# Kernel tuning notes

Hardware: AMD Instinct MI355X
Metric: run time of the kernel (lower is better)

The kernel has to match this reference:

```python
import jax, jax.numpy as jnp
import numpy as np

B, N, D, K = 8, 2048, 256, 8192


def setup_inputs() -> dict:
    key = jax.random.key(0)
    k1, k2 = jax.random.split(key)
    x = jax.random.normal(k1, (B, N, D), dtype=jnp.float32)          # encoder output z_e (identity encoder)
    codebook = jax.random.normal(k2, (K, D), dtype=jnp.float32)      # nn.Parameter(codebook_size, codebook_dim)
    return {"x": x, "codebook": codebook}


def reference(x, codebook):
    z_e = x  # identity encoder
    # Squared Euclidean distances via matmul expansion: ||z||^2 - 2 z.c^T + ||c||^2 -> (B, N, K)
    z2 = jnp.sum(z_e * z_e, axis=-1, keepdims=True)                   # (B, N, 1)
    c2 = jnp.sum(codebook * codebook, axis=-1)                        # (K,)
    cross = jnp.einsum('bnd,kd->bnk', z_e, codebook)                  # (B, N, K)
    distances = z2 - 2.0 * cross + c2                                 # (B, N, K)
    indices = jnp.argmin(distances, axis=-1)                          # (B, N) int
    z_q = codebook[indices]                                           # gather -> (B, N, D)
    x_recon = z_q  # identity decoder
    return (x_recon, z_e, z_q, indices)
```

## Files before the change

kernel.cpp:

```cpp
#include <hip/hip_runtime.h>
#include <stdint.h>


#define M_ROWS 16384
#define D_DIM  256
#define K_CB   8192
#define NSPLIT 16
#define CHUNK  64
#define EPS 20.0f

typedef float f32x4 __attribute__((ext_vector_type(4)));
typedef int   int4v __attribute__((ext_vector_type(4)));
typedef int   int8v __attribute__((ext_vector_type(8)));

__device__ __forceinline__ uint32_t umin32(uint32_t a, uint32_t b) { return a < b ? a : b; }
__device__ __forceinline__ uint32_t umax32(uint32_t a, uint32_t b) { return a > b ? a : b; }

__device__ __forceinline__ void gld_lds16(const void* g, void* l) {
  __builtin_amdgcn_global_load_lds((__attribute__((address_space(1))) void*)g,
                                   (__attribute__((address_space(3))) void*)l,
                                   16, 0, 0);
}

__device__ __forceinline__ float rtne3(float f) {
  uint32_t u = __float_as_uint(f);
  u = (u + 0x0007FFFFu + ((u >> 20) & 1u)) & 0xFFF00000u;
  return __uint_as_float(u);
}

__device__ __forceinline__ uint32_t fp8x4(const f32x4 v) {
  int p = __builtin_amdgcn_cvt_pk_fp8_f32(rtne3(v[0]), rtne3(v[1]), 0, false);
  p = __builtin_amdgcn_cvt_pk_fp8_f32(rtne3(v[2]), rtne3(v[3]), p, true);
  return (uint32_t)p;
}

__global__ __launch_bounds__(256) void prep(const float* __restrict__ x,
                                            const float* __restrict__ cb,
                                            uint8_t* __restrict__ Ap,
                                            uint8_t* __restrict__ Bp,
                                            float* __restrict__ c2s,
                                            float* __restrict__ out_ze) {
  const int w = threadIdx.x >> 6, lane = threadIdx.x & 63;
  if (blockIdx.x < M_ROWS / 4) {
    const int row = blockIdx.x * 4 + w;
    const f32x4 v = *(const f32x4*)(x + (size_t)row * D_DIM + lane * 4);
    *(uint32_t*)(Ap + (size_t)row * D_DIM + lane * 4) = fp8x4(v);
    *(f32x4*)(out_ze + (size_t)row * D_DIM + lane * 4) = v;
  } else {
    const int row = (blockIdx.x - M_ROWS / 4) * 4 + w;
    const f32x4 v = *(const f32x4*)(cb + (size_t)row * D_DIM + lane * 4);
    *(uint32_t*)(Bp + (size_t)row * D_DIM + lane * 4) = fp8x4(v);
    double s = 0.0;
#pragma unroll
    for (int t = 0; t < 4; ++t) s += (double)v[t] * (double)v[t];
#pragma unroll
    for (int m = 1; m < 64; m <<= 1) s += __shfl_xor(s, m, 64);
    if (lane == 0) c2s[row] = (float)s + 1024.0f;
  }
}

__global__ __launch_bounds__(256, 3) void vq_main(const uint8_t* __restrict__ Ap,
                                                  const uint8_t* __restrict__ Bp,
                                                  const float* __restrict__ c2s,
                                                  uint4* __restrict__ part) {
  __shared__ uint8_t Bs[2][CHUNK * D_DIM];

  const int w    = threadIdx.x >> 6;
  const int lane = threadIdx.x & 63;
  const int fr   = lane & 15;
  const int fq   = lane >> 4;

  const int rowBase = blockIdx.x * 128 + w * 32;
  const int colBase = blockIdx.y * 512;

  int8v af[2][2];
  {
    const uint8_t* ab = Ap + (size_t)(rowBase + fr) * D_DIM + fq * 32;
#pragma unroll
    for (int i = 0; i < 2; ++i)
#pragma unroll
      for (int kh = 0; kh < 2; ++kh)
        af[i][kh] = *(const int8v*)(ab + (size_t)(i * 16) * D_DIM + kh * 128);
  }

  uint32_t t1[2][4], t2[2][4], t3[2][4], t4[2][4];
#pragma unroll
  for (int i = 0; i < 2; ++i)
#pragma unroll
    for (int r = 0; r < 4; ++r) {
      t1[i][r] = 0x7f7ffe00u; t2[i][r] = 0x7f7ffe00u;
      t3[i][r] = 0x7f7ffe00u; t4[i][r] = 0x7f7ffe00u;
    }

  const int dRow = lane >> 4;
  const int dChk = lane & 15;
#define STAGE_DMA(c, buf)                                                        \
  {                                                                              \
    _Pragma("unroll")                                                            \
    for (int ii = 0; ii < 4; ++ii) {                                             \
      const int r0  = w * 16 + ii * 4;                                           \
      const int row = r0 + dRow;                                                 \
      gld_lds16(Bp + (size_t)(colBase + (c) * CHUNK + row) * D_DIM +             \
                    ((dChk ^ (row & 15)) << 4),                                  \
                &Bs[buf][r0 * D_DIM] + lane * 16);                               \
    }                                                                            \
  }

  STAGE_DMA(0, 0);

  for (int c = 0; c < 512 / CHUNK; ++c) {
    __syncthreads();
    if (c < 512 / CHUNK - 1) STAGE_DMA(c + 1, (c + 1) & 1);

    const uint8_t* bsb = Bs[c & 1];
    const int cb0 = c * CHUNK;
    float cvv[4];
#pragma unroll
    for (int jj = 0; jj < 4; ++jj)
      cvv[jj] = c2s[colBase + cb0 + jj * 16 + fr];

#pragma unroll
    for (int jj = 0; jj < 4; ++jj) {
      const uint8_t* bp = bsb + (jj * 16 + fr) * D_DIM;
      f32x4 acc[2];
      acc[0] = (f32x4){0.f, 0.f, 0.f, 0.f};
      acc[1] = (f32x4){0.f, 0.f, 0.f, 0.f};
#pragma unroll
      for (int kh = 0; kh < 2; ++kh) {
        const int L0 = kh * 8 + fq * 2;
        const int4v lo = *(const int4v*)(bp + ((L0 ^ fr) << 4));
        const int4v hi = *(const int4v*)(bp + (((L0 + 1) ^ fr) << 4));
        int8v bf;
#pragma unroll
        for (int t = 0; t < 4; ++t) { bf[t] = lo[t]; bf[4 + t] = hi[t]; }
#pragma unroll
        for (int i = 0; i < 2; ++i)
          acc[i] = __builtin_amdgcn_mfma_scale_f32_16x16x128_f8f6f4(
              af[i][kh], bf, acc[i], 0, 0,
              0, 0x7f7f7f7f, 0, 0x7f7f7f7f);
      }
      const int col9 = cb0 + jj * 16 + fr;
      const float cv = cvv[jj];
#pragma unroll
      for (int i = 0; i < 2; ++i)
#pragma unroll
        for (int r = 0; r < 4; ++r) {
          const float s = fmaf(-2.0f, acc[i][r], cv);
          const uint32_t p = (__float_as_uint(s) & ~511u) | (uint32_t)col9;
          const uint32_t b = umax32(t1[i][r], p); t1[i][r] = umin32(t1[i][r], p);
          const uint32_t d = umax32(t2[i][r], b); t2[i][r] = umin32(t2[i][r], b);
          const uint32_t f = umax32(t3[i][r], d); t3[i][r] = umin32(t3[i][r], d);
          t4[i][r] = umin32(t4[i][r], f);
        }
    }
  }

#pragma unroll
  for (int i = 0; i < 2; ++i)
#pragma unroll
    for (int r = 0; r < 4; ++r) {
      uint32_t a1 = t1[i][r], a2 = t2[i][r], a3 = t3[i][r], a4 = t4[i][r];
#pragma unroll
      for (int m = 1; m < 16; m <<= 1) {
        const uint32_t b1 = __shfl_xor(a1, m, 64);
        const uint32_t b2 = __shfl_xor(a2, m, 64);
        const uint32_t b3 = __shfl_xor(a3, m, 64);
        const uint32_t b4 = __shfl_xor(a4, m, 64);
        uint32_t c1 = umin32(a1, b4), c2_ = umin32(a2, b3);
        uint32_t c3 = umin32(a3, b2), c4 = umin32(a4, b1);
        uint32_t lo, hi;
        lo = umin32(c1, c3); hi = umax32(c1, c3); c1 = lo; c3 = hi;
        lo = umin32(c2_, c4); hi = umax32(c2_, c4); c2_ = lo; c4 = hi;
        lo = umin32(c1, c2_); hi = umax32(c1, c2_); c1 = lo; c2_ = hi;
        lo = umin32(c3, c4); hi = umax32(c3, c4); c3 = lo; c4 = hi;
        a1 = c1; a2 = c2_; a3 = c3; a4 = c4;
      }
      if (fr == 0) {
        const int row = rowBase + i * 16 + fq * 4 + r;
        part[(size_t)row * NSPLIT + blockIdx.y] = make_uint4(a1, a2, a3, a4);
      }
    }
}

__global__ __launch_bounds__(256) void vq_merge(const uint32_t* __restrict__ part,
                                                const float* __restrict__ x,
                                                const float* __restrict__ cb,
                                                float* __restrict__ out) {
  const int w = threadIdx.x >> 6, lane = threadIdx.x & 63;
  const int row = blockIdx.x * 4 + w;

  const uint32_t pk = part[(size_t)row * 64 + lane];
  const int gidx = (lane >> 2) * (K_CB / NSPLIT) + (int)(pk & 511u);

  uint32_t pmin = pk;
#pragma unroll
  for (int m = 1; m < 64; m <<= 1) {
    const uint32_t o = __shfl_xor(pmin, m, 64);
    pmin = pmin < o ? pmin : o;
  }
  const float vmin = __uint_as_float(pmin & ~511u);
  const float vme  = __uint_as_float(pk & ~511u);
  const unsigned long long mask = __ballot(vme <= vmin + EPS);

  int winner;
  if (__popcll(mask) == 1) {
    winner = __shfl(gidx, __ffsll((long long)mask) - 1, 64);
  } else {
    const f32x4 xv = *(const f32x4*)(x + (size_t)row * D_DIM + lane * 4);
    double bestd = 1.0e300;
    int bidx = 0x7fffffff;
    unsigned long long mm = mask;
    while (mm) {
      const int q = __ffsll((long long)mm) - 1;
      mm &= mm - 1;
      const int ci = __shfl(gidx, q, 64);
      const f32x4 cv = *(const f32x4*)(cb + (size_t)ci * D_DIM + lane * 4);
      double s = 0.0;
#pragma unroll
      for (int t = 0; t < 4; ++t) {
        const double dx = (double)xv[t] - (double)cv[t];
        s += dx * dx;
      }
#pragma unroll
      for (int m = 1; m < 64; m <<= 1) s += __shfl_xor(s, m, 64);
      if (s < bestd || (s == bestd && ci < bidx)) { bestd = s; bidx = ci; }
    }
    winner = bidx;
  }

  float* out_recon = out;
  float* out_zq    = out + 2 * (size_t)M_ROWS * D_DIM;
  float* out_idx   = out + 3 * (size_t)M_ROWS * D_DIM;

  const f32x4 cv = *(const f32x4*)(cb + (size_t)winner * D_DIM + lane * 4);
  *(f32x4*)(out_recon + (size_t)row * D_DIM + lane * 4) = cv;
  *(f32x4*)(out_zq    + (size_t)row * D_DIM + lane * 4) = cv;
  if (lane == 0) out_idx[row] = (float)winner;
}

extern "C" void kernel_launch(void* const* d_in, const int* in_sizes, int n_in,
                              void* d_out, int out_size, void* d_ws, size_t ws_size,
                              hipStream_t stream) {
  const float* x  = (const float*)d_in[0];
  const float* cb = (const float*)d_in[1];
  float* out = (float*)d_out;

  char* ws = (char*)d_ws;
  float*    c2s  = (float*)ws;
  uint4*    part = (uint4*)(ws + 32768);
  uint8_t*  Ap   = (uint8_t*)(ws + 32768 + 4194304);
  uint8_t*  Bp   = Ap + (size_t)M_ROWS * D_DIM;
  if (ws_size < (size_t)(32768 + 4194304 + 4194304 + 2097152 + 4096)) return;

  float* out_ze = out + (size_t)M_ROWS * D_DIM;

  prep    <<<dim3(M_ROWS / 4 + K_CB / 4), dim3(256), 0, stream>>>(x, cb, Ap, Bp, c2s, out_ze);
  vq_main <<<dim3(M_ROWS / 128, NSPLIT), dim3(256), 0, stream>>>(Ap, Bp, c2s, part);
  vq_merge<<<dim3(M_ROWS / 4), dim3(256), 0, stream>>>((const uint32_t*)part, x, cb, out);
}
```

Measured before the change: 183.9 us.

## Fold -2 scale and norm into MFMA, use med3 top-4 insert, batch rescoring

The -2 factor is folded into the fp8 quantisation of x, and the codebook norm seeds the MFMA accumulator, which removes the per-element FMA. The top-4 sorted insert now uses float min and med3 instead of umin/umax chains, cutting VALU work in the hot epilogue. DMA offsets are precomputed once per thread. The finalize rescoring now evaluates 8 candidates at a time using 8-lane groups instead of one per wave iteration. Using float med3 on the packed keys assumes the keys stay non-negative and keep their ordering, and scaling by -2 before fp8 rounding is exact because it is a power of two.

```diff
diff --git a/kernel.cpp b/kernel.cpp
--- a/kernel.cpp
+++ b/kernel.cpp
@@ -15,6 +15,14 @@
 
 __device__ __forceinline__ uint32_t umin32(uint32_t a, uint32_t b) { return a < b ? a : b; }
 __device__ __forceinline__ uint32_t umax32(uint32_t a, uint32_t b) { return a > b ? a : b; }
+
+__device__ __forceinline__ uint32_t fmin32(uint32_t a, uint32_t b) {
+  return __float_as_uint(fminf(__uint_as_float(a), __uint_as_float(b)));
+}
+__device__ __forceinline__ uint32_t fmed32(uint32_t a, uint32_t b, uint32_t c) {
+  return __float_as_uint(__builtin_amdgcn_fmed3f(
+      __uint_as_float(a), __uint_as_float(b), __uint_as_float(c)));
+}
 
 __device__ __forceinline__ void gld_lds16(const void* g, void* l) {
   __builtin_amdgcn_global_load_lds((__attribute__((address_space(1))) void*)g,
@@ -44,7 +52,10 @@
   if (blockIdx.x < M_ROWS / 4) {
     const int row = blockIdx.x * 4 + w;
     const f32x4 v = *(const f32x4*)(x + (size_t)row * D_DIM + lane * 4);
-    *(uint32_t*)(Ap + (size_t)row * D_DIM + lane * 4) = fp8x4(v);
+    f32x4 nv;
+#pragma unroll
+    for (int t = 0; t < 4; ++t) nv[t] = -2.0f * v[t];
+    *(uint32_t*)(Ap + (size_t)row * D_DIM + lane * 4) = fp8x4(nv);
     *(f32x4*)(out_ze + (size_t)row * D_DIM + lane * 4) = v;
   } else {
     const int row = (blockIdx.x - M_ROWS / 4) * 4 + w;
@@ -83,6 +94,24 @@
         af[i][kh] = *(const int8v*)(ab + (size_t)(i * 16) * D_DIM + kh * 128);
   }
 
+  const int dRow = lane >> 4;
+  const int dChk = lane & 15;
+  int goff[4];
+#pragma unroll
+  for (int ii = 0; ii < 4; ++ii) {
+    const int rr = ii * 4 + dRow;
+    goff[ii] = rr * D_DIM + ((dChk ^ rr) << 4);
+  }
+
+#define STAGE_DMA(c, buf)                                                      \
+  {                                                                            \
+    const uint8_t* gb = Bp + ((size_t)(colBase + (c) * CHUNK + w * 16) << 8);  \
+    uint8_t* lb = &Bs[buf][w * 16 * D_DIM] + lane * 16;                        \
+    _Pragma("unroll")                                                          \
+    for (int ii = 0; ii < 4; ++ii)                                             \
+      gld_lds16(gb + goff[ii], lb + ii * 4 * D_DIM);                           \
+  }
+
   uint32_t t1[2][4], t2[2][4], t3[2][4], t4[2][4];
 #pragma unroll
   for (int i = 0; i < 2; ++i)
@@ -92,19 +121,8 @@
       t3[i][r] = 0x7f7ffe00u; t4[i][r] = 0x7f7ffe00u;
     }
 
-  const int dRow = lane >> 4;
-  const int dChk = lane & 15;
-#define STAGE_DMA(c, buf)                                                        \
-  {                                                                              \
-    _Pragma("unroll")                                                            \
-    for (int ii = 0; ii < 4; ++ii) {                                             \
-      const int r0  = w * 16 + ii * 4;                                           \
-      const int row = r0 + dRow;                                                 \
-      gld_lds16(Bp + (size_t)(colBase + (c) * CHUNK + row) * D_DIM +             \
-                    ((dChk ^ (row & 15)) << 4),                                  \
-                &Bs[buf][r0 * D_DIM] + lane * 16);                               \
-    }                                                                            \
-  }
+  const float* c2p = c2s + colBase + fr;
+  const int y0 = (fq * 2) << 4;
 
   STAGE_DMA(0, 0);
 
@@ -117,19 +135,20 @@
     float cvv[4];
 #pragma unroll
     for (int jj = 0; jj < 4; ++jj)
-      cvv[jj] = c2s[colBase + cb0 + jj * 16 + fr];
+      cvv[jj] = c2p[cb0 + jj * 16];
 
 #pragma unroll
     for (int jj = 0; jj < 4; ++jj) {
       const uint8_t* bp = bsb + (jj * 16 + fr) * D_DIM;
+      const float cv = cvv[jj];
       f32x4 acc[2];
-      acc[0] = (f32x4){0.f, 0.f, 0.f, 0.f};
-      acc[1] = (f32x4){0.f, 0.f, 0.f, 0.f};
+      acc[0] = (f32x4){cv, cv, cv, cv};
+      acc[1] = (f32x4){cv, cv, cv, cv};
 #pragma unroll
       for (int kh = 0; kh < 2; ++kh) {
-        const int L0 = kh * 8 + fq * 2;
-        const int4v lo = *(const int4v*)(bp + ((L0 ^ fr) << 4));
-        const int4v hi = *(const int4v*)(bp + (((L0 + 1) ^ fr) << 4));
+        const int y = (y0 ^ (fr << 4)) ^ (kh << 7);
+        const int4v lo = *(const int4v*)(bp + y);
+        const int4v hi = *(const int4v*)(bp + (y ^ 16));
         int8v bf;
 #pragma unroll
         for (int t = 0; t < 4; ++t) { bf[t] = lo[t]; bf[4 + t] = hi[t]; }
@@ -140,17 +159,18 @@
               0, 0x7f7f7f7f, 0, 0x7f7f7f7f);
       }
       const int col9 = cb0 + jj * 16 + fr;
-      const float cv = cvv[jj];
 #pragma unroll
       for (int i = 0; i < 2; ++i)
 #pragma unroll
         for (int r = 0; r < 4; ++r) {
-          const float s = fmaf(-2.0f, acc[i][r], cv);
-          const uint32_t p = (__float_as_uint(s) & ~511u) | (uint32_t)col9;
-          const uint32_t b = umax32(t1[i][r], p); t1[i][r] = umin32(t1[i][r], p);
-          const uint32_t d = umax32(t2[i][r], b); t2[i][r] = umin32(t2[i][r], b);
-          const uint32_t f = umax32(t3[i][r], d); t3[i][r] = umin32(t3[i][r], d);
-          t4[i][r] = umin32(t4[i][r], f);
+          const uint32_t p =
+              (__float_as_uint(acc[i][r]) & ~511u) | (uint32_t)col9;
+          const uint32_t o1 = t1[i][r], o2 = t2[i][r];
+          const uint32_t o3 = t3[i][r], o4 = t4[i][r];
+          t1[i][r] = fmin32(p, o1);
+          t2[i][r] = fmed32(p, o1, o2);
+          t3[i][r] = fmed32(p, o2, o3);
+          t4[i][r] = fmed32(p, o3, o4);
         }
     }
   }
@@ -201,29 +221,50 @@
   const float vmin = __uint_as_float(pmin & ~511u);
   const float vme  = __uint_as_float(pk & ~511u);
   const unsigned long long mask = __ballot(vme <= vmin + EPS);
+  const int nq = __popcll(mask);
 
   int winner;
-  if (__popcll(mask) == 1) {
+  if (nq == 1) {
     winner = __shfl(gidx, __ffsll((long long)mask) - 1, 64);
   } else {
-    const f32x4 xv = *(const f32x4*)(x + (size_t)row * D_DIM + lane * 4);
-    double bestd = 1.0e300;
+    const int g = lane >> 3, sub = lane & 7;
+    const float* xrow = x + (size_t)row * D_DIM;
+    double best = 1.0e300;
     int bidx = 0x7fffffff;
-    unsigned long long mm = mask;
-    while (mm) {
-      const int q = __ffsll((long long)mm) - 1;
-      mm &= mm - 1;
-      const int ci = __shfl(gidx, q, 64);
-      const f32x4 cv = *(const f32x4*)(cb + (size_t)ci * D_DIM + lane * 4);
+    unsigned long long bm = mask;
+    for (int batch = 0; batch * 8 < nq; ++batch) {
+      unsigned long long mm = bm;
+#pragma unroll
+      for (int t = 0; t < 7; ++t)
+        if (t < g) mm &= mm - 1;
+      const bool valid = (batch * 8 + g) < nq;
+      const int qlane = valid ? (__ffsll((long long)mm) - 1) : 0;
+      int ci = __shfl(gidx, qlane, 64);
+      const float* cbp = cb + (size_t)ci * D_DIM;
       double s = 0.0;
 #pragma unroll
-      for (int t = 0; t < 4; ++t) {
-        const double dx = (double)xv[t] - (double)cv[t];
-        s += dx * dx;
+      for (int t = 0; t < 8; ++t) {
+        const int d = (t * 8 + sub) * 4;
+        const f32x4 xv = *(const f32x4*)(xrow + d);
+        const f32x4 cv = *(const f32x4*)(cbp + d);
+#pragma unroll
+        for (int u = 0; u < 4; ++u) {
+          const double dx = (double)xv[u] - (double)cv[u];
+          s += dx * dx;
+        }
       }
 #pragma unroll
-      for (int m = 1; m < 64; m <<= 1) s += __shfl_xor(s, m, 64);
-      if (s < bestd || (s == bestd && ci < bidx)) { bestd = s; bidx = ci; }
+      for (int m = 1; m < 8; m <<= 1) s += __shfl_xor(s, m, 64);
+      if (!valid) { s = 1.0e300; ci = 0x7fffffff; }
+      if (s < best || (s == best && ci < bidx)) { best = s; bidx = ci; }
+#pragma unroll
+      for (int t = 0; t < 8; ++t) bm &= bm - 1;
+    }
+#pragma unroll
+    for (int m = 8; m < 64; m <<= 1) {
+      const double ob = __shfl_xor(best, m, 64);
+      const int oi = __shfl_xor(bidx, m, 64);
+      if (ob < best || (ob == best && oi < bidx)) { best = ob; bidx = oi; }
     }
     winner = bidx;
   }
```

Result: faster. 179.4 us (-2.5%).
